# Kernel tuning notes

Measured on AMD Instinct MI355X. Metric: run time of the kernel, lower is better.

Reference implementation:

```python
import jax, jax.numpy as jnp
import numpy as np

EPS = 1e-8
LOG_EPS = 1e-20  # guard before log for categorical logits


def setup_inputs() -> dict:
    key = jax.random.key(0)
    B, T, K, I = 64, 1024, 512, 4
    k1, k2, k3, k4 = jax.random.split(key, 4)
    data = jax.random.randint(k1, (B, T), 0, K)
    masks = jax.random.bernoulli(k2, 0.5, (B, T)).astype(jnp.float32)
    init_p = jax.random.uniform(k3, (K,), dtype=jnp.float32)
    init_p = init_p / (init_p.sum() + EPS)
    P = jax.random.uniform(k4, (K, K), dtype=jnp.float32)
    P = P / (P.sum(axis=1, keepdims=True) + EPS)
    return {
        "data": data,
        "masks": masks,
        "init_probability": init_p,
        "transition_probability": P,
        "nb_imputation": I,
    }


def _forward_filter(data, masks, init_p, P):
    """HMM forward filtering. Returns messages [T, B, K]."""
    B, T = data.shape
    K = init_p.shape[0]
    oh = jax.nn.one_hot(data, K, dtype=init_p.dtype)      # [B,T,K]
    m = masks[..., None]                                   # [B,T,1]
    msg0 = init_p[None, :] * (1.0 - m[:, 0]) + m[:, 0] * oh[:, 0]
    msg0 = msg0 / (msg0.sum(-1, keepdims=True) + EPS)

    def step(prev, xs):
        oh_i, m_i = xs                                     # [B,K],[B,1]
        msg = (prev @ P) * (1.0 - m_i) + m_i * oh_i
        msg = msg / msg.sum(-1, keepdims=True)             # source uses no eps for t>=1
        return msg, msg

    xs = (jnp.moveaxis(oh[:, 1:], 1, 0), jnp.moveaxis(m[:, 1:], 1, 0))
    _, rest = jax.lax.scan(step, msg0, xs)                 # [T-1,B,K]
    return jnp.concatenate([msg0[None], rest], axis=0)    # [T,B,K]


def reference(data, masks, init_probability, transition_probability, nb_imputation):
    B, T = data.shape
    K = init_probability.shape[0]
    I = nb_imputation
    P = transition_probability

    messages = _forward_filter(data, masks, init_probability, P)  # [T,B,K]

    key = jax.random.key(42)
    k_last, k_seq = jax.random.split(key)

    # --- sample last timestep ---
    logp_last = jnp.log(messages[-1] + LOG_EPS)            # [B,K]
    s_last = jax.random.categorical(k_last, logp_last[:, None, :], shape=(B, I))
    m_last = masks[:, -1][:, None] > 0
    d_last = data[:, -1][:, None]
    # NOTE: faithful to source, last step uses mask*sample + (1-mask)*data
    out_last = jnp.where(m_last, s_last, d_last)           # [B,I]

    # --- backward sampling scan, t = T-2 .. 0 ---
    PT = P.T                                               # row j = P[:, j]
    keys = jax.random.split(k_seq, T - 1)

    def bstep(s_next, xs):
        msg_i, m_i, d_i, k_i = xs                          # [B,K],[B],[B],key
        trans = PT[s_next]                                 # [B,I,K] = P[:, s_next].T
        w = msg_i[:, None, :] * (trans + 1.0 / K)
        w = w / (w.sum(-1, keepdims=True) + EPS)
        s = jax.random.categorical(k_i, jnp.log(w + LOG_EPS))  # [B,I]
        # other steps: (1-mask)*sample + mask*data
        s = jnp.where(m_i[:, None] > 0, d_i[:, None], s)
        return s, s

    xs = (
        messages[: T - 1][::-1],                           # [T-1,B,K]
        masks[:, : T - 1].T[::-1],                         # [T-1,B]
        data[:, : T - 1].T[::-1],                          # [T-1,B]
        keys,
    )
    _, samples = jax.lax.scan(bstep, out_last, xs)         # [T-1,B,I] reversed time
    samples = samples[::-1]
    out = jnp.concatenate([samples, out_last[None]], axis=0)  # [T,B,I]
    return jnp.moveaxis(out, 0, 2)                         # [B,I,T]
```

## Files before the change

### kernel.cpp

```cpp
#include <hip/hip_runtime.h>
#include <stdint.h>


#define JAX_PARTITIONABLE 1

#define B_ 64
#define T_ 1024
#define K_ 512
#define I_ 4
#define NCHAIN (B_ * I_)
#define POWSLOT (513 * 512)
#define LMAX_WANT 6
#define MAXRUNS 32769
#define BWD_BLOCKS 8192
#define GEMM_BLOCKS (17 * 16)
#define SORT_BLOCKS 129

typedef double f64x4 __attribute__((ext_vector_type(4)));

__host__ __device__ inline void tf2x32(uint32_t k0, uint32_t k1, uint32_t c0, uint32_t c1,
                                       uint32_t& o0, uint32_t& o1) {
  uint32_t ks2 = k0 ^ k1 ^ 0x1BD11BDAu;
  uint32_t x0 = c0 + k0;
  uint32_t x1 = c1 + k1;
#define TFR(r) { x0 += x1; x1 = (x1 << (r)) | (x1 >> (32 - (r))); x1 ^= x0; }
  TFR(13) TFR(15) TFR(26) TFR(6)
  x0 += k1; x1 += ks2 + 1u;
  TFR(17) TFR(29) TFR(16) TFR(24)
  x0 += ks2; x1 += k0 + 2u;
  TFR(13) TFR(15) TFR(26) TFR(6)
  x0 += k0; x1 += k1 + 3u;
  TFR(17) TFR(29) TFR(16) TFR(24)
  x0 += k1; x1 += ks2 + 4u;
  TFR(13) TFR(15) TFR(26) TFR(6)
  x0 += ks2; x1 += k0 + 5u;
#undef TFR
  o0 = x0; o1 = x1;
}

__device__ inline uint32_t rng_bits(uint32_t kj0, uint32_t kj1, uint32_t e) {
#if JAX_PARTITIONABLE
  uint32_t a, b;
  tf2x32(kj0, kj1, 0u, e, a, b);
  return a ^ b;
#else
  const uint32_t HALF = (uint32_t)(NCHAIN * K_ / 2);
  uint32_t a, b;
  if (e < HALF) { tf2x32(kj0, kj1, e, e + HALF, a, b); return a; }
  else          { tf2x32(kj0, kj1, e - HALF, e, a, b); return b; }
#endif
}

__device__ inline float gumbel_scale(uint32_t bits) {
  float f = __uint_as_float((bits >> 9) | 0x3F800000u) - 1.0f;
  float u = f + 1.17549435e-38f;
  int iu = __float_as_int(u);
  float ef = (float)((iu >> 23) - 127);
  float m = __int_as_float((iu & 0x007fffff) | 0x3f800000);
  int big = m > 1.41421356f;
  m = big ? m * 0.5f : m;
  ef = big ? ef + 1.0f : ef;
  float fm = m - 1.0f;
  float r = fm * __builtin_amdgcn_rcpf(m + 1.0f);
  float r2 = r * r;
  float p = fmaf(r2, fmaf(r2, fmaf(r2, fmaf(r2, 0.11111111f, 0.14285715f),
                                   0.2f), 0.33333334f), 1.0f);
  float logu = fmaf(ef, 0.69314718f, (r + r) * p);
  return -__builtin_amdgcn_rcpf(logu);
}

__device__ inline void step_key(uint32_t ks0, uint32_t ks1, int j, uint32_t& kj0, uint32_t& kj1) {
#if JAX_PARTITIONABLE
  tf2x32(ks0, ks1, 0u, (uint32_t)j, kj0, kj1);
#else
  const int N = T_ - 1;
  uint32_t o0, o1;
  int v = 2 * j;
  if (v < N) { tf2x32(ks0, ks1, (uint32_t)v, (uint32_t)(v + N), o0, o1); kj0 = o0; }
  else       { tf2x32(ks0, ks1, (uint32_t)(v - N), (uint32_t)v, o0, o1); kj0 = o1; }
  v = 2 * j + 1;
  if (v < N) { tf2x32(ks0, ks1, (uint32_t)v, (uint32_t)(v + N), o0, o1); kj1 = o0; }
  else       { tf2x32(ks0, ks1, (uint32_t)(v - N), (uint32_t)v, o0, o1); kj1 = o1; }
#endif
}

__global__ __launch_bounds__(1024) void setup_all(
    const int* __restrict__ data, const float* __restrict__ masks,
    const float* __restrict__ P, const float* __restrict__ initp,
    float* __restrict__ POW0, float* __restrict__ PTp,
    float* __restrict__ INITROW, float* __restrict__ V1,
    int* __restrict__ off, int lmax, int initoff,
    int* __restrict__ runs, int* __restrict__ runCount, int* __restrict__ maxLdev,
    int* __restrict__ hist,
    uint32_t* __restrict__ KEY0, uint32_t* __restrict__ KEY1,
    uint32_t ks0, uint32_t ks1) {
  int blk = blockIdx.x;
  int tid = threadIdx.x;
  if (blk < 64) {
    __shared__ int prevObs[1024];
    __shared__ int nextObs[1024];
    __shared__ int lhist[64];
    __shared__ int lmaxL;
    int b = blk;
    int t = tid;
    bool obs = masks[b * T_ + t] > 0.0f;
    prevObs[t] = obs ? t : -1;
    nextObs[t] = obs ? t : T_;
    if (t < 64) lhist[t] = 0;
    if (t == 0) lmaxL = 1;
    __syncthreads();
    for (int o = 1; o < 1024; o <<= 1) {
      int pv = (t >= o) ? prevObs[t - o] : -1;
      int nv = (t + o < 1024) ? nextObs[t + o] : T_;
      __syncthreads();
      if (pv > prevObs[t]) prevObs[t] = pv;
      if (nv < nextObs[t]) nextObs[t] = nv;
      __syncthreads();
    }
    int t0 = (t > 0) ? prevObs[t - 1] : -1;
    int idx = b * T_ + t;
    if (obs) off[idx] = -1;
    else if (t0 >= 0) {
      int L = t - t0; if (L > lmax) L = lmax;
      off[idx] = (L - 1) * POWSLOT + data[b * T_ + t0] * 512;
    } else if (t == 0) off[idx] = initoff;
    else {
      int L = t; if (L > lmax) L = lmax;
      off[idx] = (L - 1) * POWSLOT + 512 * 512;
    }
    if (!obs && t <= T_ - 2 && (t == 0 || masks[b * T_ + t - 1] > 0.0f)) {
      int te = nextObs[t] - 1; if (te > T_ - 2) te = T_ - 2;
      int r = atomicAdd(runCount, 1);
      if (r < MAXRUNS) {
        runs[r] = (b << 20) | (t << 10) | te;
        int steps = te - t + 1;
        int bkt = steps < 63 ? steps : 63;
        atomicAdd(&lhist[bkt], 1);
        int maxL = (t == 0) ? te : (te - t + 1);
        if (maxL > 1) atomicMax(&lmaxL, maxL);
      }
    }
    __syncthreads();
    if (t < 64) {
      int c = lhist[t];
      if (c) atomicAdd(&hist[t], c);
    }
    if (t == 0) {
      int v = lmaxL;
      if (v > 1) atomicMax(maxLdev, v);
    }
  } else if (blk < 128) {
    __shared__ float Tls[64][65];
    int tt = blk - 64, tr = tt >> 3, tc = tt & 7;
    int r = tid >> 4, c4 = (tid & 15) << 2;
    int src = ((tr << 6) + r) * 512 + (tc << 6) + c4;
    float4 v = *(const float4*)(P + src);
    *(float4*)(POW0 + src) = v;
    Tls[c4 + 0][r] = v.x;
    Tls[c4 + 1][r] = v.y;
    Tls[c4 + 2][r] = v.z;
    Tls[c4 + 3][r] = v.w;
    __syncthreads();
    const float q = 0.001953125f;
    float4 w;
    w.x = Tls[r][c4 + 0] + q;
    w.y = Tls[r][c4 + 1] + q;
    w.z = Tls[r][c4 + 2] + q;
    w.w = Tls[r][c4 + 3] + q;
    *(float4*)(PTp + ((tc << 6) + r) * 512 + (tr << 6) + c4) = w;
  } else if (blk == 128) {
    __shared__ double vred[512];
    int c = tid & 511, h = tid >> 9;
    const float* Ph = P + h * 256 * 512;
    const float* ih = initp + h * 256;
    double acc = 0.0;
    for (int j = 0; j < 256; ++j) acc += (double)ih[j] * (double)Ph[j * 512 + c];
    if (h == 0) vred[c] = acc;
    __syncthreads();
    if (h == 1) V1[c] = (float)(vred[c] + acc);
    if (tid < 512) INITROW[tid] = initp[tid];
  } else {
    if (tid < T_ - 1) {
      uint32_t a, b;
      step_key(ks0, ks1, tid, a, b);
      KEY0[tid] = a; KEY1[tid] = b;
    }
  }
}

__global__ __launch_bounds__(256) void power_gemm_mfma(
    float* __restrict__ POW, int m, int lmax, const int* __restrict__ maxLdev,
    int sortN, const int* __restrict__ runs, const int* __restrict__ runCount,
    const int* __restrict__ hist, int* __restrict__ cursor,
    int* __restrict__ runsSorted) {
  if (blockIdx.x >= GEMM_BLOCKS) {
    if (sortN && blockIdx.y == 0) {
      __shared__ int lhist2[64];
      __shared__ int gbase[64];
      __shared__ int sbase[64];
      int tid = threadIdx.x;
      int i = (blockIdx.x - GEMM_BLOCKS) * 256 + tid;
      int total = *runCount; if (total > MAXRUNS) total = MAXRUNS;
      bool valid = i < total;
      if (tid < 64) lhist2[tid] = 0;
      __syncthreads();
      int r = 0, bkt = 0, lr = 0;
      if (valid) {
        r = runs[i];
        int ta = (r >> 10) & 1023, tb = r & 1023;
        int steps = tb - ta + 1;
        bkt = steps < 63 ? steps : 63;
        lr = atomicAdd(&lhist2[bkt], 1);
      }
      __syncthreads();
      if (tid < 64) {
        int c = lhist2[tid];
        gbase[tid] = c ? atomicAdd(&cursor[tid], c) : 0;
        int s = 0;
        for (int l = tid + 1; l < 64; ++l) s += hist[l];
        sbase[tid] = s;
      }
      __syncthreads();
      if (valid) runsSorted[sbase[bkt] + gbase[bkt] + lr] = r;
    }
    return;
  }
  int y = blockIdx.y;
  {
    int gate = *maxLdev; if (gate > lmax) gate = lmax;
    if (y + 1 + m > gate) return;
  }
  const float* A  = POW + (size_t)y * POWSLOT;
  const float* Bm = POW + (size_t)(m - 1) * POWSLOT;
  float* C        = POW + (size_t)(y + m) * POWSLOT;
  __shared__ double As[32][33];
  __shared__ double Bs[32][33];
  int tid = threadIdx.x;
  int lane = tid & 63;
  int wv = tid >> 6;
  int wr = wv >> 1, wc = wv & 1;
  int q = lane >> 4, r16 = lane & 15;
  int r0 = (blockIdx.x >> 4) * 32;
  int c0 = (blockIdx.x & 15) * 32;

  f64x4 z = {0.0, 0.0, 0.0, 0.0};
  f64x4 d1 = __builtin_amdgcn_mfma_f64_16x16x4f64((double)r16, 1.0, z, 0, 0, 0);
  f64x4 d2 = __builtin_amdgcn_mfma_f64_16x16x4f64(1.0, (double)r16, z, 0, 0, 0);
  int ir[4], ic[4];
#pragma unroll
  for (int v = 0; v < 4; ++v) {
    ir[v] = (((int)d1[v]) >> 2) & 15;
    ic[v] = (((int)d2[v]) >> 2) & 15;
  }

  int sr = tid >> 3;
  int sk4 = (tid & 7) * 4;
  int ar = r0 + sr; if (ar > 512) ar = 512;

  f64x4 acc = {0.0, 0.0, 0.0, 0.0};
  float4 av = *(const float4*)(A + (size_t)ar * 512 + sk4);
  float4 bv = *(const float4*)(Bm + (size_t)sr * 512 + c0 + sk4);
  for (int kc = 0; kc < 512; kc += 32) {
    __syncthreads();
    As[sk4 + 0][sr] = (double)av.x;
    As[sk4 + 1][sr] = (double)av.y;
    As[sk4 + 2][sr] = (double)av.z;
    As[sk4 + 3][sr] = (double)av.w;
    Bs[sr][sk4 + 0] = (double)bv.x;
    Bs[sr][sk4 + 1] = (double)bv.y;
    Bs[sr][sk4 + 2] = (double)bv.z;
    Bs[sr][sk4 + 3] = (double)bv.w;
    int kn = (kc + 32 < 512) ? kc + 32 : 480;
    av = *(const float4*)(A + (size_t)ar * 512 + kn + sk4);
    bv = *(const float4*)(Bm + (size_t)(kn + sr) * 512 + c0 + sk4);
    __syncthreads();
#pragma unroll
    for (int ks = 0; ks < 8; ++ks) {
      double a = As[ks * 4 + q][wr * 16 + r16];
      double b = Bs[ks * 4 + q][wc * 16 + r16];
      acc = __builtin_amdgcn_mfma_f64_16x16x4f64(a, b, acc, 0, 0, 0);
    }
  }
#pragma unroll
  for (int v = 0; v < 4; ++v) {
    int gr = r0 + wr * 16 + ir[v];
    int gc = c0 + wc * 16 + ic[v];
    if (gr < 513) C[(size_t)gr * 512 + gc] = (float)acc[v];
  }
}

__global__ __launch_bounds__(256) void backward_run(
    const int* __restrict__ data, const float* __restrict__ masks,
    const float* __restrict__ wsF, const int* __restrict__ off,
    const float* __restrict__ PTp,
    const uint32_t* __restrict__ KEY0, const uint32_t* __restrict__ KEY1,
    const int* __restrict__ runs, const int* __restrict__ runCount,
    int* __restrict__ out) {
  {
    int id = blockIdx.x * 256 + threadIdx.x;
    if (id < NCHAIN * T_) {
      int t = id & (T_ - 1);
      int b = id >> 12;
      if (t == T_ - 1 || masks[b * T_ + t] > 0.0f) out[id] = data[b * T_ + t];
    }
  }
  int lane = threadIdx.x & 63;
  int wv = threadIdx.x >> 6;
  int wid = blockIdx.x * 4 + wv;
  const int NW = BWD_BLOCKS * 4;
  int total = *runCount;
  if (total > MAXRUNS) total = MAXRUNS;
  total <<= 2;
  const float* wsL = wsF + (lane << 3);
  const float* ptL = PTp + (lane << 3);
  for (int u = wid; u < total; u += NW) {
    int run = runs[u >> 2];
    int ci = u & 3;
    int b = run >> 20, ta = (run >> 10) & 1023, tb = run & 1023;
    int s = data[b * T_ + tb + 1];
    uint32_t ebase = ((uint32_t)b << 11) | ((uint32_t)ci << 9) | ((uint32_t)(lane << 3));
    const int* offb = off + b * T_;
    int* outp = out + (((b << 2) | ci) * T_);
    for (int t = tb; t >= ta; --t) {
      int j = (T_ - 2) - t;
      uint32_t kj0 = KEY0[j], kj1 = KEY1[j];
      int o = offb[t];
      float4 m0 = *(const float4*)(wsL + o);
      float4 m1 = *(const float4*)(wsL + o + 4);
      const float* prow = ptL + ((size_t)s << 9);
      float4 p0 = *(const float4*)(prow);
      float4 p1 = *(const float4*)(prow + 4);
      float x0 = fmaf(m0.x, p0.x, 1e-20f) * gumbel_scale(rng_bits(kj0, kj1, ebase + 0u));
      float x1 = fmaf(m0.y, p0.y, 1e-20f) * gumbel_scale(rng_bits(kj0, kj1, ebase + 1u));
      float x2 = fmaf(m0.z, p0.z, 1e-20f) * gumbel_scale(rng_bits(kj0, kj1, ebase + 2u));
      float x3 = fmaf(m0.w, p0.w, 1e-20f) * gumbel_scale(rng_bits(kj0, kj1, ebase + 3u));
      float x4 = fmaf(m1.x, p1.x, 1e-20f) * gumbel_scale(rng_bits(kj0, kj1, ebase + 4u));
      float x5 = fmaf(m1.y, p1.y, 1e-20f) * gumbel_scale(rng_bits(kj0, kj1, ebase + 5u));
      float x6 = fmaf(m1.z, p1.z, 1e-20f) * gumbel_scale(rng_bits(kj0, kj1, ebase + 6u));
      float x7 = fmaf(m1.w, p1.w, 1e-20f) * gumbel_scale(rng_bits(kj0, kj1, ebase + 7u));
      float bv = x0; int bj = 0;
      if (x1 > bv) { bv = x1; bj = 1; }
      if (x2 > bv) { bv = x2; bj = 2; }
      if (x3 > bv) { bv = x3; bj = 3; }
      if (x4 > bv) { bv = x4; bj = 4; }
      if (x5 > bv) { bv = x5; bj = 5; }
      if (x6 > bv) { bv = x6; bj = 6; }
      if (x7 > bv) { bv = x7; bj = 7; }
      float wm = bv;
#pragma unroll
      for (int d = 1; d < 64; d <<= 1) wm = fmaxf(wm, __shfl_xor(wm, d));
      unsigned long long bal = __ballot(bv == wm);
      int wl = __ffsll(bal) - 1;
      int jw = __shfl(bj, wl);
      s = (wl << 3) + jw;
      if (lane == 0) outp[t] = s;
    }
  }
}

extern "C" void kernel_launch(void* const* d_in, const int* in_sizes, int n_in,
                              void* d_out, int out_size, void* d_ws, size_t ws_size,
                              hipStream_t stream) {
  const int* data = (const int*)d_in[0];
  const float* masks = (const float*)d_in[1];
  const float* initp = (const float*)d_in[2];
  const float* P = (const float*)d_in[3];
  int* out = (int*)d_out;

  int lmax = LMAX_WANT;
  {
    long long fixed = 512LL * 512 + 512 + (long long)B_ * T_ + 2 * (T_ - 1)
                      + 2LL * MAXRUNS + 256;
    long long avail = (long long)(ws_size / 4) - fixed;
    long long fit = avail / POWSLOT;
    if (fit < lmax) lmax = (fit < 1) ? 1 : (int)fit;
  }
  float* wsF = (float*)d_ws;
  float* POW = wsF;
  float* PTp = wsF + (size_t)lmax * POWSLOT;
  float* INITROW = PTp + 512 * 512;
  int* off = (int*)(INITROW + 512);
  uint32_t* KEY0 = (uint32_t*)(off + B_ * T_);
  uint32_t* KEY1 = KEY0 + (T_ - 1);
  int* runs = (int*)(KEY1 + (T_ - 1));
  int* runCount = runs + MAXRUNS;
  int* maxLdev = runCount + 1;
  int* histcur = runCount + 2;
  int* hist = histcur;
  int* cursor = histcur + 64;
  int* runsSorted = histcur + 128;
  int initoff = lmax * POWSLOT + 512 * 512;

  uint32_t ks0, ks1;
#if JAX_PARTITIONABLE
  tf2x32(0u, 42u, 0u, 1u, ks0, ks1);
#else
  {
    uint32_t a0, b0, a1, b1;
    tf2x32(0u, 42u, 0u, 2u, a0, b0);
    tf2x32(0u, 42u, 1u, 3u, a1, b1);
    ks0 = b0; ks1 = b1;
  }
#endif

  hipMemsetAsync(runCount, 0, 130 * sizeof(int), stream);
  hipLaunchKernelGGL(setup_all, dim3(130), dim3(1024), 0, stream,
                     data, masks, P, initp, POW, PTp, INITROW, POW + 512 * 512,
                     off, lmax, initoff, runs, runCount, maxLdev, hist,
                     KEY0, KEY1, ks0, ks1);
  int m = 1, first = 1;
  while (m < lmax) {
    int count = lmax - m; if (count > m) count = m;
    hipLaunchKernelGGL(power_gemm_mfma,
                       dim3(GEMM_BLOCKS + (first ? SORT_BLOCKS : 0), count), dim3(256), 0, stream,
                       POW, m, lmax, maxLdev,
                       first, runs, runCount, hist, cursor, runsSorted);
    first = 0;
    m += count;
  }
  if (first) {
    hipLaunchKernelGGL(power_gemm_mfma,
                       dim3(GEMM_BLOCKS + SORT_BLOCKS, 1), dim3(256), 0, stream,
                       POW, 1, lmax, maxLdev,
                       1, runs, runCount, hist, cursor, runsSorted);
  }
  hipLaunchKernelGGL(backward_run, dim3(BWD_BLOCKS), dim3(256), 0, stream,
                     data, masks, wsF, off, PTp, KEY0, KEY1, runsSorted, runCount, out);
}
```

Baseline: 299.7 us.

## Fold first matrix-power GEMM into setup kernel and use ballot-based gap scan

Result: no change. 294.9 us (-1.6%).

```diff
diff --git a/kernel.cpp b/kernel.cpp
--- a/kernel.cpp
+++ b/kernel.cpp
@@ -15,6 +15,7 @@
 #define BWD_BLOCKS 8192
 #define GEMM_BLOCKS (17 * 16)
 #define SORT_BLOCKS 129
+#define SETUP_GEMM_TILES 256
 
 typedef double f64x4 __attribute__((ext_vector_type(4)));
 
@@ -84,165 +85,14 @@
 #endif
 }
 
-__global__ __launch_bounds__(1024) void setup_all(
-    const int* __restrict__ data, const float* __restrict__ masks,
-    const float* __restrict__ P, const float* __restrict__ initp,
-    float* __restrict__ POW0, float* __restrict__ PTp,
-    float* __restrict__ INITROW, float* __restrict__ V1,
-    int* __restrict__ off, int lmax, int initoff,
-    int* __restrict__ runs, int* __restrict__ runCount, int* __restrict__ maxLdev,
-    int* __restrict__ hist,
-    uint32_t* __restrict__ KEY0, uint32_t* __restrict__ KEY1,
-    uint32_t ks0, uint32_t ks1) {
-  int blk = blockIdx.x;
-  int tid = threadIdx.x;
-  if (blk < 64) {
-    __shared__ int prevObs[1024];
-    __shared__ int nextObs[1024];
-    __shared__ int lhist[64];
-    __shared__ int lmaxL;
-    int b = blk;
-    int t = tid;
-    bool obs = masks[b * T_ + t] > 0.0f;
-    prevObs[t] = obs ? t : -1;
-    nextObs[t] = obs ? t : T_;
-    if (t < 64) lhist[t] = 0;
-    if (t == 0) lmaxL = 1;
-    __syncthreads();
-    for (int o = 1; o < 1024; o <<= 1) {
-      int pv = (t >= o) ? prevObs[t - o] : -1;
-      int nv = (t + o < 1024) ? nextObs[t + o] : T_;
-      __syncthreads();
-      if (pv > prevObs[t]) prevObs[t] = pv;
-      if (nv < nextObs[t]) nextObs[t] = nv;
-      __syncthreads();
-    }
-    int t0 = (t > 0) ? prevObs[t - 1] : -1;
-    int idx = b * T_ + t;
-    if (obs) off[idx] = -1;
-    else if (t0 >= 0) {
-      int L = t - t0; if (L > lmax) L = lmax;
-      off[idx] = (L - 1) * POWSLOT + data[b * T_ + t0] * 512;
-    } else if (t == 0) off[idx] = initoff;
-    else {
-      int L = t; if (L > lmax) L = lmax;
-      off[idx] = (L - 1) * POWSLOT + 512 * 512;
-    }
-    if (!obs && t <= T_ - 2 && (t == 0 || masks[b * T_ + t - 1] > 0.0f)) {
-      int te = nextObs[t] - 1; if (te > T_ - 2) te = T_ - 2;
-      int r = atomicAdd(runCount, 1);
-      if (r < MAXRUNS) {
-        runs[r] = (b << 20) | (t << 10) | te;
-        int steps = te - t + 1;
-        int bkt = steps < 63 ? steps : 63;
-        atomicAdd(&lhist[bkt], 1);
-        int maxL = (t == 0) ? te : (te - t + 1);
-        if (maxL > 1) atomicMax(&lmaxL, maxL);
-      }
-    }
-    __syncthreads();
-    if (t < 64) {
-      int c = lhist[t];
-      if (c) atomicAdd(&hist[t], c);
-    }
-    if (t == 0) {
-      int v = lmaxL;
-      if (v > 1) atomicMax(maxLdev, v);
-    }
-  } else if (blk < 128) {
-    __shared__ float Tls[64][65];
-    int tt = blk - 64, tr = tt >> 3, tc = tt & 7;
-    int r = tid >> 4, c4 = (tid & 15) << 2;
-    int src = ((tr << 6) + r) * 512 + (tc << 6) + c4;
-    float4 v = *(const float4*)(P + src);
-    *(float4*)(POW0 + src) = v;
-    Tls[c4 + 0][r] = v.x;
-    Tls[c4 + 1][r] = v.y;
-    Tls[c4 + 2][r] = v.z;
-    Tls[c4 + 3][r] = v.w;
-    __syncthreads();
-    const float q = 0.001953125f;
-    float4 w;
-    w.x = Tls[r][c4 + 0] + q;
-    w.y = Tls[r][c4 + 1] + q;
-    w.z = Tls[r][c4 + 2] + q;
-    w.w = Tls[r][c4 + 3] + q;
-    *(float4*)(PTp + ((tc << 6) + r) * 512 + (tr << 6) + c4) = w;
-  } else if (blk == 128) {
-    __shared__ double vred[512];
-    int c = tid & 511, h = tid >> 9;
-    const float* Ph = P + h * 256 * 512;
-    const float* ih = initp + h * 256;
-    double acc = 0.0;
-    for (int j = 0; j < 256; ++j) acc += (double)ih[j] * (double)Ph[j * 512 + c];
-    if (h == 0) vred[c] = acc;
-    __syncthreads();
-    if (h == 1) V1[c] = (float)(vred[c] + acc);
-    if (tid < 512) INITROW[tid] = initp[tid];
-  } else {
-    if (tid < T_ - 1) {
-      uint32_t a, b;
-      step_key(ks0, ks1, tid, a, b);
-      KEY0[tid] = a; KEY1[tid] = b;
-    }
-  }
-}
-
-__global__ __launch_bounds__(256) void power_gemm_mfma(
-    float* __restrict__ POW, int m, int lmax, const int* __restrict__ maxLdev,
-    int sortN, const int* __restrict__ runs, const int* __restrict__ runCount,
-    const int* __restrict__ hist, int* __restrict__ cursor,
-    int* __restrict__ runsSorted) {
-  if (blockIdx.x >= GEMM_BLOCKS) {
-    if (sortN && blockIdx.y == 0) {
-      __shared__ int lhist2[64];
-      __shared__ int gbase[64];
-      __shared__ int sbase[64];
-      int tid = threadIdx.x;
-      int i = (blockIdx.x - GEMM_BLOCKS) * 256 + tid;
-      int total = *runCount; if (total > MAXRUNS) total = MAXRUNS;
-      bool valid = i < total;
-      if (tid < 64) lhist2[tid] = 0;
-      __syncthreads();
-      int r = 0, bkt = 0, lr = 0;
-      if (valid) {
-        r = runs[i];
-        int ta = (r >> 10) & 1023, tb = r & 1023;
-        int steps = tb - ta + 1;
-        bkt = steps < 63 ? steps : 63;
-        lr = atomicAdd(&lhist2[bkt], 1);
-      }
-      __syncthreads();
-      if (tid < 64) {
-        int c = lhist2[tid];
-        gbase[tid] = c ? atomicAdd(&cursor[tid], c) : 0;
-        int s = 0;
-        for (int l = tid + 1; l < 64; ++l) s += hist[l];
-        sbase[tid] = s;
-      }
-      __syncthreads();
-      if (valid) runsSorted[sbase[bkt] + gbase[bkt] + lr] = r;
-    }
-    return;
-  }
-  int y = blockIdx.y;
-  {
-    int gate = *maxLdev; if (gate > lmax) gate = lmax;
-    if (y + 1 + m > gate) return;
-  }
-  const float* A  = POW + (size_t)y * POWSLOT;
-  const float* Bm = POW + (size_t)(m - 1) * POWSLOT;
-  float* C        = POW + (size_t)(y + m) * POWSLOT;
-  __shared__ double As[32][33];
-  __shared__ double Bs[32][33];
-  int tid = threadIdx.x;
+__device__ __forceinline__ void gemm_tile_core(
+    const float* __restrict__ A, const float* __restrict__ Bm, float* __restrict__ C,
+    int r0, int c0, int maxRowA, int writeRows,
+    double (*As)[33], double (*Bs)[33], int tid) {
   int lane = tid & 63;
   int wv = tid >> 6;
   int wr = wv >> 1, wc = wv & 1;
   int q = lane >> 4, r16 = lane & 15;
-  int r0 = (blockIdx.x >> 4) * 32;
-  int c0 = (blockIdx.x & 15) * 32;
-
   f64x4 z = {0.0, 0.0, 0.0, 0.0};
   f64x4 d1 = __builtin_amdgcn_mfma_f64_16x16x4f64((double)r16, 1.0, z, 0, 0, 0);
   f64x4 d2 = __builtin_amdgcn_mfma_f64_16x16x4f64(1.0, (double)r16, z, 0, 0, 0);
@@ -252,11 +102,9 @@
     ir[v] = (((int)d1[v]) >> 2) & 15;
     ic[v] = (((int)d2[v]) >> 2) & 15;
   }
-
   int sr = tid >> 3;
   int sk4 = (tid & 7) * 4;
-  int ar = r0 + sr; if (ar > 512) ar = 512;
-
+  int ar = r0 + sr; if (ar > maxRowA) ar = maxRowA;
   f64x4 acc = {0.0, 0.0, 0.0, 0.0};
   float4 av = *(const float4*)(A + (size_t)ar * 512 + sk4);
   float4 bv = *(const float4*)(Bm + (size_t)sr * 512 + c0 + sk4);
@@ -285,8 +133,196 @@
   for (int v = 0; v < 4; ++v) {
     int gr = r0 + wr * 16 + ir[v];
     int gc = c0 + wc * 16 + ic[v];
-    if (gr < 513) C[(size_t)gr * 512 + gc] = (float)acc[v];
-  }
+    if (gr < writeRows) C[(size_t)gr * 512 + gc] = (float)acc[v];
+  }
+}
+
+__global__ __launch_bounds__(1024) void setup_all(
+    const int* __restrict__ data, const float* __restrict__ masks,
+    const float* __restrict__ P, const float* __restrict__ initp,
+    float* __restrict__ POW0, float* __restrict__ PTp,
+    float* __restrict__ INITROW, float* __restrict__ V1,
+    int* __restrict__ off, int lmax, int initoff,
+    int* __restrict__ runs, int* __restrict__ runCount, int* __restrict__ maxLdev,
+    int* __restrict__ hist,
+    uint32_t* __restrict__ KEY0, uint32_t* __restrict__ KEY1,
+    uint32_t ks0, uint32_t ks1) {
+  __shared__ double smem[2112];
+  int blk = blockIdx.x;
+  int tid = threadIdx.x;
+  if (blk < 64) {
+    unsigned long long* wmask = (unsigned long long*)smem;
+    int* pIncl = (int*)(smem + 16);
+    int* lhist = (int*)(smem + 528);
+    int* lmaxL = (int*)(smem + 560);
+    int b = blk, t = tid, l = t & 63, w = t >> 6;
+    bool obs = masks[b * T_ + t] > 0.0f;
+    unsigned long long mw = __ballot(obs);
+    if (l == 0) wmask[w] = mw;
+    if (t < 64) lhist[t] = 0;
+    if (t == 0) *lmaxL = 1;
+    __syncthreads();
+    unsigned long long below = mw & (~0ull >> (63 - l));
+    int pv;
+    if (below) pv = (w << 6) + 63 - __builtin_clzll(below);
+    else {
+      pv = -1;
+      for (int w2 = w - 1; w2 >= 0; --w2) {
+        unsigned long long m2 = wmask[w2];
+        if (m2) { pv = (w2 << 6) + 63 - __builtin_clzll(m2); break; }
+      }
+    }
+    pIncl[t] = pv;
+    unsigned long long above = mw & (~0ull << l);
+    int nv;
+    if (above) nv = (w << 6) + __builtin_ctzll(above);
+    else {
+      nv = T_;
+      for (int w2 = w + 1; w2 < 16; ++w2) {
+        unsigned long long m2 = wmask[w2];
+        if (m2) { nv = (w2 << 6) + __builtin_ctzll(m2); break; }
+      }
+    }
+    __syncthreads();
+    int t0 = (t > 0) ? pIncl[t - 1] : -1;
+    int idx = b * T_ + t;
+    if (obs) off[idx] = -1;
+    else if (t0 >= 0) {
+      int L = t - t0; if (L > lmax) L = lmax;
+      off[idx] = (L - 1) * POWSLOT + data[b * T_ + t0] * 512;
+    } else if (t == 0) off[idx] = initoff;
+    else {
+      int L = t; if (L > lmax) L = lmax;
+      off[idx] = (L - 1) * POWSLOT + 512 * 512;
+    }
+    if (!obs && t <= T_ - 2 && (t == 0 || masks[b * T_ + t - 1] > 0.0f)) {
+      int te = nv - 1; if (te > T_ - 2) te = T_ - 2;
+      int r = atomicAdd(runCount, 1);
+      if (r < MAXRUNS) {
+        runs[r] = (b << 20) | (t << 10) | te;
+        int steps = te - t + 1;
+        int bkt = steps < 63 ? steps : 63;
+        atomicAdd(&lhist[bkt], 1);
+        int maxL = (t == 0) ? te : (te - t + 1);
+        if (maxL > 1) atomicMax(lmaxL, maxL);
+      }
+    }
+    __syncthreads();
+    if (t < 64) {
+      int c = lhist[t];
+      if (c) atomicAdd(&hist[t], c);
+    }
+    if (t == 0) {
+      int v = *lmaxL;
+      if (v > 1) atomicMax(maxLdev, v);
+    }
+  } else if (blk < 128) {
+    float (*Tls)[65] = (float(*)[65])smem;
+    int tt = blk - 64, tr = tt >> 3, tc = tt & 7;
+    int r = tid >> 4, c4 = (tid & 15) << 2;
+    int src = ((tr << 6) + r) * 512 + (tc << 6) + c4;
+    float4 v = *(const float4*)(P + src);
+    *(float4*)(POW0 + src) = v;
+    Tls[c4 + 0][r] = v.x;
+    Tls[c4 + 1][r] = v.y;
+    Tls[c4 + 2][r] = v.z;
+    Tls[c4 + 3][r] = v.w;
+    __syncthreads();
+    const float q = 0.001953125f;
+    float4 w;
+    w.x = Tls[r][c4 + 0] + q;
+    w.y = Tls[r][c4 + 1] + q;
+    w.z = Tls[r][c4 + 2] + q;
+    w.w = Tls[r][c4 + 3] + q;
+    *(float4*)(PTp + ((tc << 6) + r) * 512 + (tr << 6) + c4) = w;
+  } else if (blk == 128) {
+    double* vred = smem;
+    float* v1sh = (float*)(smem + 512);
+    int c = tid & 511, h = tid >> 9;
+    const float* Ph = P + h * 256 * 512;
+    const float* ih = initp + h * 256;
+    double acc = 0.0;
+    for (int j = 0; j < 256; ++j) acc += (double)ih[j] * (double)Ph[j * 512 + c];
+    if (h == 0) vred[c] = acc;
+    __syncthreads();
+    if (h == 1) {
+      float v = (float)(vred[c] + acc);
+      V1[c] = v;
+      v1sh[c] = v;
+    }
+    if (tid < 512) INITROW[tid] = initp[tid];
+    if (lmax >= 2) {
+      __syncthreads();
+      double a2 = 0.0;
+      const float* vh = v1sh + h * 256;
+      for (int j = 0; j < 256; ++j) a2 += (double)vh[j] * (double)Ph[j * 512 + c];
+      if (h == 0) vred[c] = a2;
+      __syncthreads();
+      if (h == 1) POW0[POWSLOT + 512 * 512 + c] = (float)(vred[c] + a2);
+    }
+  } else if (blk == 129) {
+    if (tid < T_ - 1) {
+      uint32_t a, b;
+      step_key(ks0, ks1, tid, a, b);
+      KEY0[tid] = a; KEY1[tid] = b;
+    }
+  } else {
+    if (lmax < 2) return;
+    if (tid >= 256) return;
+    double (*As)[33] = (double(*)[33])smem;
+    double (*Bs)[33] = (double(*)[33])(smem + 1056);
+    int tx = blk - 130;
+    gemm_tile_core(P, P, POW0 + POWSLOT, (tx >> 4) * 32, (tx & 15) * 32,
+                   511, 512, As, Bs, tid);
+  }
+}
+
+__global__ __launch_bounds__(256) void power_gemm_mfma(
+    float* __restrict__ POW, int m, int lmax, const int* __restrict__ maxLdev,
+    int sortN, const int* __restrict__ runs, const int* __restrict__ runCount,
+    const int* __restrict__ hist, int* __restrict__ cursor,
+    int* __restrict__ runsSorted) {
+  __shared__ double As[32][33];
+  __shared__ double Bs[32][33];
+  if (blockIdx.x >= GEMM_BLOCKS) {
+    if (sortN && blockIdx.y == 0) {
+      int* ish = (int*)As;
+      int tid = threadIdx.x;
+      int i = (blockIdx.x - GEMM_BLOCKS) * 256 + tid;
+      int total = *runCount; if (total > MAXRUNS) total = MAXRUNS;
+      bool valid = i < total;
+      if (tid < 64) ish[tid] = 0;
+      __syncthreads();
+      int r = 0, bkt = 0, lr = 0;
+      if (valid) {
+        r = runs[i];
+        int ta = (r >> 10) & 1023, tb = r & 1023;
+        int steps = tb - ta + 1;
+        bkt = steps < 63 ? steps : 63;
+        lr = atomicAdd(&ish[bkt], 1);
+      }
+      __syncthreads();
+      if (tid < 64) {
+        int c = ish[tid];
+        ish[64 + tid] = c ? atomicAdd(&cursor[tid], c) : 0;
+        int s = 0;
+        for (int l = tid + 1; l < 64; ++l) s += hist[l];
+        ish[128 + tid] = s;
+      }
+      __syncthreads();
+      if (valid) runsSorted[ish[128 + bkt] + ish[64 + bkt] + lr] = r;
+    }
+    return;
+  }
+  int y = blockIdx.y;
+  {
+    int gate = *maxLdev; if (gate > lmax) gate = lmax;
+    if (y + 1 + m > gate) return;
+  }
+  gemm_tile_core(POW + (size_t)y * POWSLOT, POW + (size_t)(m - 1) * POWSLOT,
+                 POW + (size_t)(y + m) * POWSLOT,
+                 (blockIdx.x >> 4) * 32, (blockIdx.x & 15) * 32,
+                 512, 513, As, Bs, threadIdx.x);
 }
 
 __global__ __launch_bounds__(256) void backward_run(
@@ -385,10 +421,9 @@
   int* runs = (int*)(KEY1 + (T_ - 1));
   int* runCount = runs + MAXRUNS;
   int* maxLdev = runCount + 1;
-  int* histcur = runCount + 2;
-  int* hist = histcur;
-  int* cursor = histcur + 64;
-  int* runsSorted = histcur + 128;
+  int* hist = runCount + 2;
+  int* cursor = runCount + 66;
+  int* runsSorted = runCount + 130;
   int initoff = lmax * POWSLOT + 512 * 512;
 
   uint32_t ks0, ks1;
@@ -404,11 +439,11 @@
 #endif
 
   hipMemsetAsync(runCount, 0, 130 * sizeof(int), stream);
-  hipLaunchKernelGGL(setup_all, dim3(130), dim3(1024), 0, stream,
+  hipLaunchKernelGGL(setup_all, dim3(130 + SETUP_GEMM_TILES), dim3(1024), 0, stream,
                      data, masks, P, initp, POW, PTp, INITROW, POW + 512 * 512,
                      off, lmax, initoff, runs, runCount, maxLdev, hist,
                      KEY0, KEY1, ks0, ks1);
-  int m = 1, first = 1;
+  int m = 2, first = 1;
   while (m < lmax) {
     int count = lmax - m; if (count > m) count = m;
     hipLaunchKernelGGL(power_gemm_mfma,
@@ -421,7 +456,7 @@
   if (first) {
     hipLaunchKernelGGL(power_gemm_mfma,
                        dim3(GEMM_BLOCKS + SORT_BLOCKS, 1), dim3(256), 0, stream,
-                       POW, 1, lmax, maxLdev,
+                       POW, 2, lmax, maxLdev,
                        1, runs, runCount, hist, cursor, runsSorted);
   }
   hipLaunchKernelGGL(backward_run, dim3(BWD_BLOCKS), dim3(256), 0, stream,
```
